# Optimization experiments

Hardware: AMD Instinct MI355X
Metric: run time of the kernel (lower is better)

The kernel has to match this reference:

```python
import jax, jax.numpy as jnp
import numpy as np

N_NODES = 50000
N_EDGES = 800000
IN_DIM = 128
OUT_DIM = 128
NEG_INIT = -1e9  # matches torch fill_(-1e9) init for scatter amax
LEAKY_SLOPE = 0.01  # nn.LeakyReLU default


def setup_inputs() -> dict:
    key = jax.random.key(0)
    ks = jax.random.split(key, 8)
    x = jax.random.normal(ks[0], (N_NODES, IN_DIM), dtype=jnp.float32)
    edge_index = jax.random.randint(ks[1], (2, N_EDGES), 0, N_NODES, dtype=jnp.int64)
    edge_weight = jax.random.uniform(ks[2], (N_EDGES,), dtype=jnp.float32)
    # MLP params (nn.Linear default init: U(-1/sqrt(fan_in), 1/sqrt(fan_in)))
    s1 = 1.0 / np.sqrt(IN_DIM)
    s2 = 1.0 / np.sqrt(OUT_DIM)
    w1 = jax.random.uniform(ks[3], (OUT_DIM, IN_DIM), minval=-s1, maxval=s1, dtype=jnp.float32)
    b1 = jax.random.uniform(ks[4], (OUT_DIM,), minval=-s1, maxval=s1, dtype=jnp.float32)
    w2 = jax.random.uniform(ks[5], (OUT_DIM, OUT_DIM), minval=-s2, maxval=s2, dtype=jnp.float32)
    b2 = jax.random.uniform(ks[6], (OUT_DIM,), minval=-s2, maxval=s2, dtype=jnp.float32)
    eps = jnp.zeros((1,), dtype=jnp.float32)
    return {"x": x, "edge_index": edge_index, "edge_weight": edge_weight,
            "w1": w1, "b1": b1, "w2": w2, "b2": b2, "eps": eps}


def reference(x, edge_index, edge_weight, w1, b1, w2, b2, eps):
    src = edge_index[0]
    dst = edge_index[1]
    # gather + optional edge-weight scale: [E, D]
    messages = x[src] * edge_weight[:, None]
    # scatter-max to dst; init at -1e9 so include_self=False semantics hold
    agg = jnp.full(x.shape, NEG_INIT, dtype=x.dtype).at[dst].max(messages)
    agg = jnp.where(agg == NEG_INIT, jnp.zeros_like(agg), agg)  # isolated nodes -> 0
    h = (1.0 + eps) * x + agg  # eps broadcasts ([1])
    h = h @ w1.T + b1
    h = jnp.where(h >= 0, h, LEAKY_SLOPE * h)  # LeakyReLU
    out = h @ w2.T + b2
    return out
```

## Files before the change

### kernel.cpp

```cpp
#include <hip/hip_runtime.h>
#include <stdint.h>

#define NN 50000
#define NE 800000
#define D  128
#define CAP 64
#define OVF_CAP 131072

#define CNT_OFF     64
#define OVF_CNT_OFF (CNT_OFF + NN)
#define OVF_OFF     (OVF_CNT_OFF + 4)
#define BKT_OFF     312320
#define XH_OFF      (BKT_OFF + NN * CAP)
#define WH_OFF      (XH_OFF + 65536 * (D / 2))

#define HSTRIDE 136
#define SLOTS   24
#define WLDS    (SLOTS * 256 + 1024)

#define FILL_BLKS 3125
#define PX_BLKS   6250
#define PW_BLKS   32

typedef _Float16 half8 __attribute__((ext_vector_type(8)));
typedef __attribute__((ext_vector_type(4))) float float4v;

__device__ __forceinline__ float b2f(uint16_t u) {
    union { uint32_t u; float f; } v; v.u = ((uint32_t)u) << 16; return v.f;
}
__device__ __forceinline__ uint16_t f2b(float f) {
    union { float f; uint32_t u; } v; v.f = f;
    uint32_t r = v.u + 0x7fffu + ((v.u >> 16) & 1u);
    return (uint16_t)(r >> 16);
}
__device__ __forceinline__ ushort f2h(float f) {
    union { _Float16 h; ushort u; } v; v.h = (_Float16)f; return v.u;
}
__device__ __forceinline__ float h2f(ushort u) {
    union { ushort u; _Float16 h; } v; v.u = u; return (float)v.h;
}

__device__ __forceinline__ void gload_lds4(const void* g, void* l) {
    __builtin_amdgcn_global_load_lds(
        (const __attribute__((address_space(1))) void*)g,
        (__attribute__((address_space(3))) void*)l, 4, 0, 0);
}

__device__ __forceinline__ void block_probe(const uint16_t* __restrict__ xraw,
                                            const int* __restrict__ eraw,
                                            int* sflags) {
    int t = threadIdx.x;
    if (t < 64) {
        float v0 = b2f(xraw[2 * t]);
        float v1 = b2f(xraw[2 * t + 1]);
        int bad = (!(v0 > -1e4f && v0 < 1e4f)) || (!(v1 > -1e4f && v1 < 1e4f));
        unsigned long long bm = __ballot(bad);
        int nz = (t < 32) ? (eraw[2 * t + 1] != 0) : 0;
        unsigned long long im = __ballot(nz);
        if (t == 0) { sflags[0] = bm ? 1 : 0; sflags[1] = im ? 0 : 1; }
    }
    __syncthreads();
}

__global__ __launch_bounds__(256) void prep_fill_kernel(
    const uint16_t* __restrict__ xraw,
    const int*      __restrict__ eraw,
    const uint16_t* __restrict__ ewraw,
    const uint16_t* __restrict__ w1raw,
    const uint16_t* __restrict__ w2raw,
    int* __restrict__ ws)
{
    __shared__ int sflags[2];
    block_probe(xraw, eraw, sflags);
    const int f32 = sflags[0], i64 = sflags[1];

    int bid = blockIdx.x;
    if (bid < FILL_BLKS) {
        int e = bid * 256 + threadIdx.x;
        int src, dst;
        if (i64) {
            const long long* e64 = (const long long*)eraw;
            src = (int)e64[e];
            dst = (int)e64[NE + e];
        } else {
            src = eraw[e];
            dst = eraw[NE + e];
        }
        if ((unsigned)src >= NN || (unsigned)dst >= NN) return;
        uint w = f32 ? (uint)f2h(((const float*)ewraw)[e]) : (uint)f2h(b2f(ewraw[e]));
        uint entry = (w << 16) | (uint)src;
        int slot = atomicAdd(ws + CNT_OFF + dst, 1) + 1;
        if (slot < CAP) {
            ((uint*)(ws + BKT_OFF))[(size_t)dst * CAP + slot] = entry;
        } else {
            int o = atomicAdd(ws + OVF_CNT_OFF, 1) + 1;
            if (o < OVF_CAP) {
                ws[OVF_OFF + 2 * o]     = dst;
                ws[OVF_OFF + 2 * o + 1] = (int)entry;
            }
        }
    } else if (bid < FILL_BLKS + PX_BLKS) {
        int i4 = ((bid - FILL_BLKS) * 256 + threadIdx.x) * 4;
        ushort* dst = (ushort*)(ws + XH_OFF);
        if (f32) {
            float4 v = *(const float4*)((const float*)xraw + i4);
            ushort4 o; o.x = f2h(v.x); o.y = f2h(v.y); o.z = f2h(v.z); o.w = f2h(v.w);
            *(ushort4*)(dst + i4) = o;
        } else {
            ushort4 v = *(const ushort4*)(xraw + i4);
            ushort4 o; o.x = f2h(b2f(v.x)); o.y = f2h(b2f(v.y));
            o.z = f2h(b2f(v.z)); o.w = f2h(b2f(v.w));
            *(ushort4*)(dst + i4) = o;
        }
    } else {
        int i4 = ((bid - FILL_BLKS - PX_BLKS) * 256 + threadIdx.x) * 4;
        const uint16_t* src = (i4 < 16384) ? w1raw : w2raw;
        int off = i4 & 16383;
        ushort* dst = (ushort*)(ws + WH_OFF);
        if (f32) {
            float4 v = *(const float4*)((const float*)src + off);
            ushort4 o; o.x = f2h(v.x); o.y = f2h(v.y); o.z = f2h(v.z); o.w = f2h(v.w);
            *(ushort4*)(dst + i4) = o;
        } else {
            ushort4 v = *(const ushort4*)(src + off);
            ushort4 o; o.x = f2h(b2f(v.x)); o.y = f2h(b2f(v.y));
            o.z = f2h(b2f(v.z)); o.w = f2h(b2f(v.w));
            *(ushort4*)(dst + i4) = o;
        }
    }
}

__global__ __launch_bounds__(256, 4) void gmlp_kernel(
    const uint16_t* __restrict__ xraw,
    const int*      __restrict__ eraw,
    const uint16_t* __restrict__ b1raw,
    const uint16_t* __restrict__ b2raw,
    const uint16_t* __restrict__ epsraw,
    const int* __restrict__ ws,
    uint16_t* __restrict__ outraw)
{
    __shared__ char smem[4][WLDS];
    __shared__ uint tl[16 * (HSTRIDE / 2)];
    __shared__ int  sflags[2];
    ushort* hl = (ushort*)&smem[0][0];

    const int tid  = threadIdx.x;
    const int wave = tid >> 6;
    const int lane = tid & 63;
    const int m    = lane & 15;
    const int quad = lane >> 4;
    const int node0 = blockIdx.x * 16;

    const ushort* w1h = (const ushort*)(ws + WH_OFF);
    const ushort* w2h = w1h + 16384;
    const uint*   xh  = (const uint*)(ws + XH_OFF);
    const char*   xhb = (const char*)xh;
    const uint*   bkt = (const uint*)(ws + BKT_OFF);
    const uint    lane4 = (uint)lane * 4;
    char*         wbuf  = smem[wave];

    #pragma unroll
    for (int j = 0; j < 4; ++j)
        gload_lds4(bkt + (size_t)(node0 + wave * 4 + j) * CAP + lane,
                   wbuf + SLOTS * 256 + j * 256);

    int deg[4];
    uint xv[4];
    #pragma unroll
    for (int j = 0; j < 4; ++j) {
        deg[j] = ws[CNT_OFF + node0 + wave * 4 + j] + 1;
        xv[j]  = xh[(size_t)(node0 + wave * 4 + j) * 64 + lane];
    }

    block_probe(xraw, eraw, sflags);
    const int f32 = sflags[0];
    const float eps1 = 1.0f + (f32 ? ((const float*)epsraw)[0] : b2f(epsraw[0]));

    asm volatile("s_waitcnt vmcnt(0)" ::: "memory");

    #pragma unroll
    for (int j = 0; j < 4; ++j) {
        int nl = wave * 4 + j;
        int n  = node0 + nl;
        int cnt = (deg[j] < CAP) ? deg[j] : CAP;
        const uint* ewp = (const uint*)(wbuf + SLOTS * 256 + j * 256);

        asm volatile("s_waitcnt lgkmcnt(0)" ::: "memory");

        uint eq[SLOTS];
        #pragma unroll
        for (int g = 0; g < SLOTS / 4; ++g) {
            uint4 e4 = *(const uint4*)(ewp + g * 4);
            #pragma unroll
            for (int t = 0; t < 4; ++t) {
                int u = g * 4 + t;
                uint e0 = (u < cnt) ? ((const uint*)&e4)[t] : 0xffffffffu;
                eq[u] = e0;
                gload_lds4(xhb + ((e0 & 0xffffu) << 8) + lane4, wbuf + u * 256);
            }
        }
        asm volatile("s_waitcnt vmcnt(0)" ::: "memory");

        uint mm[4] = {~0u, ~0u, ~0u, ~0u};
        #pragma unroll
        for (int u = 0; u < SLOTS; ++u) {
            uint v = *(const uint*)(wbuf + u * 256 + lane4);
            uint p;
            asm("v_pk_mul_f16 %0, %1, %2 op_sel:[0,1] op_sel_hi:[1,1]"
                : "=v"(p) : "v"(v), "v"(eq[u]));
            asm("v_pk_max_f16 %0, %0, %1" : "+v"(mm[u & 3]) : "v"(p));
        }
        for (int i = SLOTS; i < cnt; ++i) {
            uint e0 = ewp[i];
            uint v  = *(const uint*)(xhb + ((e0 & 0xffffu) << 8) + lane4);
            uint p;
            asm("v_pk_mul_f16 %0, %1, %2 op_sel:[0,1] op_sel_hi:[1,1]"
                : "=v"(p) : "v"(v), "v"(e0));
            asm("v_pk_max_f16 %0, %0, %1" : "+v"(mm[0]) : "v"(p));
        }

        asm("v_pk_max_f16 %0, %0, %1" : "+v"(mm[0]) : "v"(mm[1]));
        asm("v_pk_max_f16 %0, %0, %1" : "+v"(mm[2]) : "v"(mm[3]));
        asm("v_pk_max_f16 %0, %0, %1" : "+v"(mm[0]) : "v"(mm[2]));
        float mx = h2f((ushort)(mm[0] & 0xffffu));
        float my = h2f((ushort)(mm[0] >> 16));

        if (deg[j] > CAP) {
            int novf = ws[OVF_CNT_OFF] + 1;
            if (novf > OVF_CAP) novf = OVF_CAP;
            for (int o = 0; o < novf; ++o) {
                if (ws[OVF_OFF + 2 * o] == n) {
                    uint e0 = (uint)ws[OVF_OFF + 2 * o + 1];
                    uint v  = xh[(e0 & 0xffffu) * 64 + lane];
                    float w = h2f((ushort)(e0 >> 16));
                    mx = fmaxf(mx, h2f((ushort)(v & 0xffffu)) * w);
                    my = fmaxf(my, h2f((ushort)(v >> 16)) * w);
                }
            }
        }
        if (deg[j] == 0) { mx = 0.f; my = 0.f; }

        float t0 = eps1 * h2f((ushort)(xv[j] & 0xffffu)) + mx;
        float t1 = eps1 * h2f((ushort)(xv[j] >> 16)) + my;
        tl[nl * (HSTRIDE / 2) + lane] = (uint)f2h(t0) | ((uint)f2h(t1) << 16);
    }
    __syncthreads();

    half8 a[4];
    {
        const ushort* arow = (const ushort*)tl + m * HSTRIDE + quad * 8;
        #pragma unroll
        for (int kb = 0; kb < 4; ++kb) a[kb] = *(const half8*)(arow + kb * 32);
    }

    #pragma unroll
    for (int t = 0; t < 2; ++t) {
        int ct = wave * 2 + t;
        float4v c = {0.f, 0.f, 0.f, 0.f};
        const ushort* brow = w1h + (size_t)(ct * 16 + m) * 128 + quad * 8;
        #pragma unroll
        for (int kb = 0; kb < 4; ++kb)
            c = __builtin_amdgcn_mfma_f32_16x16x32_f16(a[kb], *(const half8*)(brow + kb * 32), c, 0, 0, 0);
        float bias = f32 ? ((const float*)b1raw)[ct * 16 + m] : b2f(b1raw[ct * 16 + m]);
        #pragma unroll
        for (int r = 0; r < 4; ++r) {
            float v = c[r] + bias;
            v = (v >= 0.f) ? v : 0.01f * v;
            hl[(quad * 4 + r) * HSTRIDE + ct * 16 + m] = f2h(v);
        }
    }
    __syncthreads();

    half8 ah[4];
    {
        const ushort* hrow = hl + m * HSTRIDE + quad * 8;
        #pragma unroll
        for (int kb = 0; kb < 4; ++kb) ah[kb] = *(const half8*)(hrow + kb * 32);
    }

    #pragma unroll
    for (int t = 0; t < 2; ++t) {
        int ct = wave * 2 + t;
        float4v c = {0.f, 0.f, 0.f, 0.f};
        const ushort* brow = w2h + (size_t)(ct * 16 + m) * 128 + quad * 8;
        #pragma unroll
        for (int kb = 0; kb < 4; ++kb)
            c = __builtin_amdgcn_mfma_f32_16x16x32_f16(ah[kb], *(const half8*)(brow + kb * 32), c, 0, 0, 0);
        float bias = f32 ? ((const float*)b2raw)[ct * 16 + m] : b2f(b2raw[ct * 16 + m]);
        #pragma unroll
        for (int r = 0; r < 4; ++r) {
            float v = c[r] + bias;
            size_t o = (size_t)(node0 + quad * 4 + r) * 128 + ct * 16 + m;
            if (f32) ((float*)outraw)[o] = v;
            else     outraw[o] = f2b(v);
        }
    }
}

extern "C" void kernel_launch(void* const* d_in, const int* in_sizes, int n_in,
                              void* d_out, int out_size, void* d_ws, size_t ws_size,
                              hipStream_t stream) {
    const uint16_t* x    = (const uint16_t*)d_in[0];
    const int*      eidx = (const int*)     d_in[1];
    const uint16_t* ew   = (const uint16_t*)d_in[2];
    const uint16_t* w1   = (const uint16_t*)d_in[3];
    const uint16_t* b1   = (const uint16_t*)d_in[4];
    const uint16_t* w2   = (const uint16_t*)d_in[5];
    const uint16_t* b2   = (const uint16_t*)d_in[6];
    const uint16_t* eps  = (const uint16_t*)d_in[7];
    uint16_t*       out  = (uint16_t*)d_out;
    int* ws = (int*)d_ws;

    hipMemsetAsync((char*)d_ws + (size_t)CNT_OFF * 4, 0xFF,
                   (size_t)(NN + 1) * 4, stream);
    prep_fill_kernel<<<FILL_BLKS + PX_BLKS + PW_BLKS, 256, 0, stream>>>(
        x, eidx, ew, w1, w2, ws);
    gmlp_kernel<<<NN / 16, 256, 0, stream>>>(x, eidx, b1, b2, eps, ws, out);
}
```

Before: 196.2 us.

## Use 16-byte global-to-LDS loads for neighbor gathers and split wait

```diff
diff --git a/kernel.cpp b/kernel.cpp
--- a/kernel.cpp
+++ b/kernel.cpp
@@ -40,10 +40,10 @@
     union { ushort u; _Float16 h; } v; v.u = u; return (float)v.h;
 }
 
-__device__ __forceinline__ void gload_lds4(const void* g, void* l) {
+__device__ __forceinline__ void gload_lds16(const void* g, void* l) {
     __builtin_amdgcn_global_load_lds(
         (const __attribute__((address_space(1))) void*)g,
-        (__attribute__((address_space(3))) void*)l, 4, 0, 0);
+        (__attribute__((address_space(3))) void*)l, 16, 0, 0);
 }
 
 __device__ __forceinline__ void block_probe(const uint16_t* __restrict__ xraw,
@@ -157,12 +157,11 @@
     const char*   xhb = (const char*)xh;
     const uint*   bkt = (const uint*)(ws + BKT_OFF);
     const uint    lane4 = (uint)lane * 4;
+    const uint    sub16 = (uint)(lane & 15) * 16;
     char*         wbuf  = smem[wave];
 
-    #pragma unroll
-    for (int j = 0; j < 4; ++j)
-        gload_lds4(bkt + (size_t)(node0 + wave * 4 + j) * CAP + lane,
-                   wbuf + SLOTS * 256 + j * 256);
+    gload_lds16((const char*)(bkt + (size_t)(node0 + wave * 4) * CAP) + (uint)lane * 16,
+                wbuf + SLOTS * 256);
 
     int deg[4];
     uint xv[4];
@@ -187,28 +186,45 @@
 
         asm volatile("s_waitcnt lgkmcnt(0)" ::: "memory");
 
-        uint eq[SLOTS];
         #pragma unroll
         for (int g = 0; g < SLOTS / 4; ++g) {
+            uint slot = (uint)(g * 4) + (uint)(lane >> 4);
+            uint e0 = ewp[slot];
+            e0 = (slot < (uint)cnt) ? e0 : 0xffffffffu;
+            gload_lds16(xhb + ((e0 & 0xffffu) << 8) + sub16, wbuf + g * 1024);
+        }
+
+        uint mm[4] = {~0u, ~0u, ~0u, ~0u};
+
+        asm volatile("s_waitcnt vmcnt(3)" ::: "memory");
+        #pragma unroll
+        for (int g = 0; g < 3; ++g) {
             uint4 e4 = *(const uint4*)(ewp + g * 4);
             #pragma unroll
             for (int t = 0; t < 4; ++t) {
                 int u = g * 4 + t;
                 uint e0 = (u < cnt) ? ((const uint*)&e4)[t] : 0xffffffffu;
-                eq[u] = e0;
-                gload_lds4(xhb + ((e0 & 0xffffu) << 8) + lane4, wbuf + u * 256);
+                uint v = *(const uint*)(wbuf + u * 256 + lane4);
+                uint p;
+                asm("v_pk_mul_f16 %0, %1, %2 op_sel:[0,1] op_sel_hi:[1,1]"
+                    : "=v"(p) : "v"(v), "v"(e0));
+                asm("v_pk_max_f16 %0, %0, %1" : "+v"(mm[u & 3]) : "v"(p));
             }
         }
         asm volatile("s_waitcnt vmcnt(0)" ::: "memory");
-
-        uint mm[4] = {~0u, ~0u, ~0u, ~0u};
-        #pragma unroll
-        for (int u = 0; u < SLOTS; ++u) {
-            uint v = *(const uint*)(wbuf + u * 256 + lane4);
-            uint p;
-            asm("v_pk_mul_f16 %0, %1, %2 op_sel:[0,1] op_sel_hi:[1,1]"
-                : "=v"(p) : "v"(v), "v"(eq[u]));
-            asm("v_pk_max_f16 %0, %0, %1" : "+v"(mm[u & 3]) : "v"(p));
+        #pragma unroll
+        for (int g = 3; g < SLOTS / 4; ++g) {
+            uint4 e4 = *(const uint4*)(ewp + g * 4);
+            #pragma unroll
+            for (int t = 0; t < 4; ++t) {
+                int u = g * 4 + t;
+                uint e0 = (u < cnt) ? ((const uint*)&e4)[t] : 0xffffffffu;
+                uint v = *(const uint*)(wbuf + u * 256 + lane4);
+                uint p;
+                asm("v_pk_mul_f16 %0, %1, %2 op_sel:[0,1] op_sel_hi:[1,1]"
+                    : "=v"(p) : "v"(v), "v"(e0));
+                asm("v_pk_max_f16 %0, %0, %1" : "+v"(mm[u & 3]) : "v"(p));
+            }
         }
         for (int i = SLOTS; i < cnt; ++i) {
             uint e0 = ewp[i];
```

Measured after the change: 206.1 us. 5.1% more time.
